# Kernel tuning notes

Measured on AMD Instinct MI355X. Metric: run time of the kernel, lower is better.

Reference implementation:

```python
import jax, jax.numpy as jnp
import numpy as np

DELTA = 2.5749
BN_EPS = 1e-5
N_LAYERS = 5


def _gin_pna_conv(x, src, dst, nW1, nb1, nW2, nb2, mW, mb):
    # x: [N, D]; src/dst: [E]
    N = x.shape[0]
    msgs = x[src]                                   # [E, D] gather (message = x_j)
    cnt = jax.ops.segment_sum(jnp.ones_like(dst, dtype=x.dtype), dst, num_segments=N)  # [N]
    c = jnp.maximum(cnt, 1.0)[:, None]              # guard isolated nodes
    sums = jax.ops.segment_sum(msgs, dst, num_segments=N)          # [N, D]
    maxs = jax.ops.segment_max(msgs, dst, num_segments=N)
    maxs = jnp.where(cnt[:, None] > 0, maxs, 0.0)   # empty segments -> 0 (torch_scatter behavior)
    means = sums / c
    sq_means = jax.ops.segment_sum(msgs * msgs, dst, num_segments=N) / c
    var = jax.nn.relu(sq_means - means * means)
    base = jnp.concatenate([sums, maxs, means, var], axis=1)        # [N, 4D]
    amp = (c / DELTA) * base                        # amplification scaler
    att = (DELTA / c) * base                        # attenuation scaler
    comb = jnp.concatenate([base, amp, att], axis=1)                # [N, 12D]
    agg = comb @ mW.T + mb                          # mlp: 12D -> D
    h = agg + x                                     # GIN: (1+eps)*x_r + aggr, eps=0
    h = jax.nn.relu(h @ nW1.T + nb1) @ nW2.T + nb2  # nn = Linear-ReLU-Linear
    return h


def _batchnorm(x, gamma, beta):
    mu = jnp.mean(x, axis=0)
    var = jnp.var(x, axis=0)
    return (x - mu) * jax.lax.rsqrt(var + BN_EPS) * gamma + beta


def setup_inputs() -> dict:
    key = jax.random.key(0)
    ks = jax.random.split(key, 12)
    N, E, D, G, OUT = 100000, 1600000, 64, 512, 16
    s = 0.05
    p = lambda k, shape: jax.random.normal(k, shape, dtype=jnp.float32) * s
    return {
        "x": jax.random.normal(ks[0], (N, D), dtype=jnp.float32),
        "edge_index": jax.random.randint(ks[1], (2, E), 0, N),
        "batch": jnp.sort(jax.random.randint(ks[2], (N,), 0, G)),
        "encW": p(ks[3], (D, D)), "encb": jnp.zeros((D,), jnp.float32),
        "nnW1": p(ks[4], (N_LAYERS, D, D)), "nnb1": jnp.zeros((N_LAYERS, D), jnp.float32),
        "nnW2": p(ks[5], (N_LAYERS, D, D)), "nnb2": jnp.zeros((N_LAYERS, D), jnp.float32),
        "mlpW": p(ks[6], (N_LAYERS, D, 12 * D)), "mlpb": jnp.zeros((N_LAYERS, D), jnp.float32),
        "bnG": jnp.ones((N_LAYERS, D), jnp.float32), "bnB": jnp.zeros((N_LAYERS, D), jnp.float32),
        "fc1W": p(ks[7], (D, D)), "fc1b": jnp.zeros((D,), jnp.float32),
        "fc2W": p(ks[8], (OUT, D)), "fc2b": jnp.zeros((OUT,), jnp.float32),
    }


def reference(x, edge_index, batch, encW, encb, nnW1, nnb1, nnW2, nnb2,
              mlpW, mlpb, bnG, bnB, fc1W, fc1b, fc2W, fc2b):
    NUM_GRAPHS = 512
    src, dst = edge_index[0], edge_index[1]
    h = x @ encW.T + encb                           # encoder
    for i in range(N_LAYERS):                       # fixed small layer loop
        h = jax.nn.relu(_gin_pna_conv(h, src, dst, nnW1[i], nnb1[i],
                                      nnW2[i], nnb2[i], mlpW[i], mlpb[i]))
        h = _batchnorm(h, bnG[i], bnB[i])
    g = jax.ops.segment_sum(h, batch, num_segments=NUM_GRAPHS)      # global_add_pool
    g = jax.nn.relu(g @ fc1W.T + fc1b)              # dropout is identity in eval mode
    return g @ fc2W.T + fc2b
```

## Files before the change

### kernel.cpp

```cpp
#include <hip/hip_runtime.h>
#include <hip/hip_bf16.h>
#include <hip/hip_fp16.h>

#define DELTA 2.5749f
#define BN_EPS 1e-5f

#define NBUCK 512
#define NBLK 128
#define ECAP 3584

typedef __attribute__((ext_vector_type(8))) _Float16 f16x8;
typedef __attribute__((ext_vector_type(2))) _Float16 f16x2;
typedef __attribute__((ext_vector_type(4))) float f32x4;

__device__ inline unsigned short f2h(float f) {
    union { _Float16 h; unsigned short u; } v;
    v.h = (_Float16)f;
    return v.u;
}


__global__ __launch_bounds__(256) void k_cnt(const int* __restrict__ dst,
                                             int* __restrict__ cnts,
                                             int E, int npb, int CS) {
    __shared__ int hist[NBUCK];
    int t = threadIdx.x;
    hist[t] = 0; hist[t + 256] = 0;
    __syncthreads();
    int s0 = blockIdx.x * CS, s1 = min(s0 + CS, E);
    for (int e = s0 + t; e < s1; e += 256)
        atomicAdd(&hist[dst[e] / npb], 1);
    __syncthreads();
    cnts[blockIdx.x * NBUCK + t] = hist[t];
    cnts[blockIdx.x * NBUCK + t + 256] = hist[t + 256];
}

__global__ void k_bscan1(const int* __restrict__ cnts, int* __restrict__ bases,
                         int* __restrict__ btot) {
    __shared__ int s[NBLK];
    int b = blockIdx.x, t = threadIdx.x;
    int v = cnts[t * NBUCK + b];
    s[t] = v; __syncthreads();
    for (int off = 1; off < NBLK; off <<= 1) {
        int x = (t >= off) ? s[t - off] : 0;
        __syncthreads();
        s[t] += x;
        __syncthreads();
    }
    bases[t * NBUCK + b] = s[t] - v;
    if (t == NBLK - 1) btot[b] = s[t];
}

__global__ void k_btops(const int* __restrict__ btot, int* __restrict__ bbase,
                        int* __restrict__ rowptr, int E, int N) {
    __shared__ int s[NBUCK];
    int t = threadIdx.x;
    int v = btot[t];
    s[t] = v; __syncthreads();
    for (int off = 1; off < NBUCK; off <<= 1) {
        int x = (t >= off) ? s[t - off] : 0;
        __syncthreads();
        s[t] += x;
        __syncthreads();
    }
    bbase[t] = s[t] - v;
    if (t == 0) rowptr[N] = E;
}

__global__ __launch_bounds__(256) void k_scat(const int* __restrict__ dst,
                                              const int* __restrict__ src,
                                              const int* __restrict__ bases,
                                              const int* __restrict__ bbase,
                                              int2* __restrict__ eDS,
                                              int E, int npb, int CS) {
    __shared__ int cur[NBUCK];
    int t = threadIdx.x;
    cur[t] = bbase[t] + bases[blockIdx.x * NBUCK + t];
    cur[t + 256] = bbase[t + 256] + bases[blockIdx.x * NBUCK + t + 256];
    __syncthreads();
    int s0 = blockIdx.x * CS, s1 = min(s0 + CS, E);
    for (int e = s0 + t; e < s1; e += 256) {
        int d = dst[e];
        int p = d / npb;
        int pos = atomicAdd(&cur[p], 1);
        eDS[pos] = make_int2(d, src[e]);
    }
}

__global__ __launch_bounds__(256) void k_csr(const int2* __restrict__ eDS,
                                             const int* __restrict__ bbase,
                                             const int* __restrict__ btot,
                                             int* __restrict__ rowptr,
                                             int* __restrict__ col,
                                             float* __restrict__ cnt,
                                             int npb, int N) {
    __shared__ int2 sE[ECAP];
    __shared__ int pre[256], sc[256];
    int b = blockIdx.x, t = threadIdx.x;
    int lo = b * npb;
    if (lo >= N) return;
    int nn = min(npb, N - lo);
    int base = bbase[b], n = btot[b];
    pre[t] = 0;
    __syncthreads();
    const int2* gE = eDS + base;
    for (int i = t; i < n; i += 256) {
        int2 e = gE[i];
        if (i < ECAP) sE[i] = e;
        atomicAdd(&pre[e.x - lo], 1);
    }
    __syncthreads();
    int deg = (t < nn) ? pre[t] : 0;
    sc[t] = deg; __syncthreads();
    for (int off = 1; off < 256; off <<= 1) {
        int x = (t >= off) ? sc[t - off] : 0;
        __syncthreads();
        sc[t] += x;
        __syncthreads();
    }
    int excl = sc[t] - deg;
    if (t < nn) {
        rowptr[lo + t] = base + excl;
        cnt[lo + t] = (float)(deg > 0 ? deg : 1);
    }
    __syncthreads();
    pre[t] = excl;
    __syncthreads();
    for (int i = t; i < n; i += 256) {
        int2 e = (i < ECAP) ? sE[i] : gE[i];
        int pos = atomicAdd(&pre[e.x - lo], 1);
        col[base + pos] = e.y;
    }
}

__global__ void k_castw_mlp(const float* __restrict__ w, unsigned short* __restrict__ o,
                            int total) {
    int i = blockIdx.x * 256 + threadIdx.x;
    if (i >= total) return;
    int lane = i & 63;
    int sc = (i >> 6) & 7;
    int tile = (i >> 9) % 12;
    int layer = i / (64 * 8 * 12);
    int r16 = lane & 15, quad = lane >> 4;
    int mat = tile >> 2, nt = tile & 3;
    const float* sp = w + (size_t)(layer * 64 + nt * 16 + r16) * 768
                        + mat * 256 + sc * 32 + quad * 8;
    unsigned short* op = o + (size_t)i * 8;
#pragma unroll
    for (int j = 0; j < 8; j++) op[j] = f2h(sp[j]);
}

__global__ void k_castw_nn(const float* __restrict__ w, unsigned short* __restrict__ o,
                           int total) {
    int i = blockIdx.x * 256 + threadIdx.x;
    if (i >= total) return;
    int lane = i & 63;
    int s = (i >> 6) & 1;
    int nt = (i >> 7) & 3;
    int layer = i >> 9;
    int r16 = lane & 15, quad = lane >> 4;
    const float* sp = w + (size_t)(layer * 64 + nt * 16 + r16) * 64 + s * 32 + quad * 8;
    unsigned short* op = o + (size_t)i * 8;
#pragma unroll
    for (int j = 0; j < 8; j++) op[j] = f2h(sp[j]);
}

#define ACC2(V)                                                            \
    do {                                                                   \
        mx = __builtin_elementwise_max(mx, V);                             \
        float x0 = (float)V[0], x1 = (float)V[1];                          \
        sa += x0; qa = fmaf(x0, x0, qa);                                   \
        sb += x1; qb = fmaf(x1, x1, qb);                                   \
    } while (0)

__global__ __launch_bounds__(256) void k_agg(const unsigned short* __restrict__ h16,
                                             const int* __restrict__ rowptr,
                                             const int* __restrict__ col,
                                             const float* __restrict__ bnstat,
                                             const float* __restrict__ gamma,
                                             const float* __restrict__ beta,
                                             float invN, int first,
                                             unsigned short* __restrict__ baseF,
                                             int N) {
    int t = threadIdx.x;
    int lane = t & 63;
    int half = lane >> 5;
    int fl = lane & 31;
    int node = blockIdx.x * 8 + (t >> 6) * 2 + half;
    if (node >= N) return;
    int fo2 = fl * 2;
    float scx, scy, shx, shy;
    if (first) {
        scx = 1.f; scy = 1.f; shx = 0.f; shy = 0.f;
    } else {
        float mu0 = bnstat[fo2] * invN, mu1 = bnstat[fo2 + 1] * invN;
        float v0 = bnstat[64 + fo2] * invN - mu0 * mu0;
        float v1 = bnstat[64 + fo2 + 1] * invN - mu1 * mu1;
        scx = rsqrtf(v0 + BN_EPS) * gamma[fo2];
        scy = rsqrtf(v1 + BN_EPS) * gamma[fo2 + 1];
        shx = beta[fo2] - mu0 * scx;
        shy = beta[fo2 + 1] - mu1 * scy;
    }
    const _Float16* hp = (const _Float16*)h16;
    int s0 = rowptr[node], s1 = rowptr[node + 1];
    int deg = s1 - s0;
    float sa = 0.f, sb = 0.f, qa = 0.f, qb = 0.f;
    f16x2 mx;
    mx[0] = (_Float16)(-65504.0f); mx[1] = (_Float16)(-65504.0f);
    const _Float16* hb = hp + fo2;
    int nfull = deg >> 3;

    f16x2 vA[8];
    int cN[8];
    if (nfull >= 1) {
        int cC[8];
        const int* cp = col + s0;
#pragma unroll
        for (int j = 0; j < 8; j++) cC[j] = cp[j];
        if (nfull >= 2) {
#pragma unroll
            for (int j = 0; j < 8; j++) cN[j] = cp[8 + j];
        }
#pragma unroll
        for (int j = 0; j < 8; j++) vA[j] = *(const f16x2*)(hb + ((size_t)(unsigned)cC[j] << 6));
    }
    for (int b = 1; b < nfull; b++) {
        int cNN[8];
        f16x2 vB[8];
        if (b + 1 < nfull) {
            const int* cp = col + s0 + (b + 1) * 8;
#pragma unroll
            for (int j = 0; j < 8; j++) cNN[j] = cp[j];
        }
#pragma unroll
        for (int j = 0; j < 8; j++) vB[j] = *(const f16x2*)(hb + ((size_t)(unsigned)cN[j] << 6));
#pragma unroll
        for (int j = 0; j < 8; j++) ACC2(vA[j]);
#pragma unroll
        for (int j = 0; j < 8; j++) { vA[j] = vB[j]; }
#pragma unroll
        for (int j = 0; j < 8; j++) { cN[j] = cNN[j]; }
    }
    if (nfull >= 1) {
#pragma unroll
        for (int j = 0; j < 8; j++) ACC2(vA[j]);
    }
    int tb = s0 + nfull * 8;
    int rem = s1 - tb;
    if (rem > 0) {
        int cT[8];
        f16x2 vT[8];
#pragma unroll
        for (int j = 0; j < 8; j++) {
            int idx = (tb + j < s1) ? (tb + j) : (s1 - 1);
            cT[j] = col[idx];
        }
#pragma unroll
        for (int j = 0; j < 8; j++) vT[j] = *(const f16x2*)(hb + ((size_t)(unsigned)cT[j] << 6));
#pragma unroll
        for (int j = 0; j < 8; j++) {
            if (j < rem) ACC2(vT[j]);
        }
    }

    float c = (float)(deg > 0 ? deg : 1);
    float ic = 1.f / c;
    float sum0, sum1, max0, max1, mean0, mean1, var0, var1;
    if (deg == 0) {
        sum0 = sum1 = max0 = max1 = mean0 = mean1 = var0 = var1 = 0.f;
    } else {
        sum0 = fmaf(scx, sa, c * shx);
        sum1 = fmaf(scy, sb, c * shy);
        max0 = fmaf(scx, (float)mx[0], shx);
        max1 = fmaf(scy, (float)mx[1], shy);
        float m0 = sa * ic, m1 = sb * ic;
        mean0 = fmaf(scx, m0, shx);
        mean1 = fmaf(scy, m1, shy);
        var0 = scx * scx * fmaxf(fmaf(-m0, m0, qa * ic), 0.f);
        var1 = scy * scy * fmaxf(fmaf(-m1, m1, qb * ic), 0.f);
    }
    size_t b = (size_t)node * 256 + fo2;
    ushort2 o;
    o.x = f2h(sum0); o.y = f2h(sum1);  *(ushort2*)(baseF + b) = o;
    o.x = f2h(max0); o.y = f2h(max1);  *(ushort2*)(baseF + b + 64) = o;
    o.x = f2h(mean0); o.y = f2h(mean1); *(ushort2*)(baseF + b + 128) = o;
    o.x = f2h(var0); o.y = f2h(var1);  *(ushort2*)(baseF + b + 192) = o;
}

__global__ __launch_bounds__(256) void k_mlp(const unsigned short* __restrict__ baseF,
                                             const float* __restrict__ cnt,
                                             const unsigned short* __restrict__ mW2,
                                             const float* __restrict__ mb,
                                             const unsigned short* __restrict__ hres16,
                                             const float* __restrict__ bnstatPrev,
                                             const float* __restrict__ gammaP,
                                             const float* __restrict__ betaP,
                                             float invN, int first,
                                             const unsigned short* __restrict__ w1F,
                                             const float* __restrict__ b1,
                                             const unsigned short* __restrict__ w2F,
                                             const float* __restrict__ b2,
                                             float* __restrict__ bnstat,
                                             unsigned short* __restrict__ hOut16, int N) {
    __shared__ char smem[36864];
    _Float16* bufA = (_Float16*)smem;
    _Float16* bufB = bufA + 128 * 72;
    float* red = (float*)bufB;

    int t = threadIdx.x;
    int wave = t >> 6, lane = t & 63;
    int r16 = lane & 15, quad = lane >> 4;
    int n0 = blockIdx.x * 128;
    int m0 = n0 + wave * 32;

    const _Float16* aptr0 = (const _Float16*)baseF + (size_t)(m0 + r16) * 256 + quad * 8;
    const _Float16* aptr1 = aptr0 + 16 * 256;
    const _Float16* mw = (const _Float16*)mW2 + lane * 8;
    f32x4 acc0[12], acc1[12];
#pragma unroll
    for (int i = 0; i < 12; i++) {
        acc0[i] = (f32x4){0.f, 0.f, 0.f, 0.f};
        acc1[i] = (f32x4){0.f, 0.f, 0.f, 0.f};
    }
    f16x8 aC0 = *(const f16x8*)(aptr0);
    f16x8 aC1 = *(const f16x8*)(aptr1);

#pragma unroll 1
    for (int sc = 0; sc < 8; sc++) {
        f16x8 aN0, aN1;
        if (sc < 7) {
            aN0 = *(const f16x8*)(aptr0 + (sc + 1) * 32);
            aN1 = *(const f16x8*)(aptr1 + (sc + 1) * 32);
        }
#pragma unroll
        for (int tile = 0; tile < 12; tile++) {
            f16x8 wB = *(const f16x8*)(mw + (tile * 8 + sc) * 512);
            acc0[tile] = __builtin_amdgcn_mfma_f32_16x16x32_f16(aC0, wB, acc0[tile], 0, 0, 0);
            acc1[tile] = __builtin_amdgcn_mfma_f32_16x16x32_f16(aC1, wB, acc1[tile], 0, 0, 0);
        }
        aC0 = aN0; aC1 = aN1;
    }

    {
        int nl = wave * 32 + (lane >> 1);
        int fo = (lane & 1) * 32;
        int gn = n0 + nl;
        uint4* dp = (uint4*)(bufA + nl * 72 + fo);
        if (gn < N) {
            const uint4* sp = (const uint4*)(hres16 + (size_t)gn * 64 + fo);
            dp[0] = sp[0]; dp[1] = sp[1]; dp[2] = sp[2]; dp[3] = sp[3];
        } else {
            uint4 z = make_uint4(0, 0, 0, 0);
            dp[0] = z; dp[1] = z; dp[2] = z; dp[3] = z;
        }
    }
    __builtin_amdgcn_wave_barrier();

    float scf[4], shf[4], mbv[4];
#pragma unroll
    for (int nt = 0; nt < 4; nt++) {
        int f = nt * 16 + r16;
        mbv[nt] = mb[f];
        if (first) {
            scf[nt] = 1.f; shf[nt] = 0.f;
        } else {
            float mu = bnstatPrev[f] * invN;
            float var = bnstatPrev[64 + f] * invN - mu * mu;
            float s = rsqrtf(var + BN_EPS) * gammaP[f];
            scf[nt] = s; shf[nt] = betaP[f] - mu * s;
        }
    }
#pragma unroll
    for (int mt = 0; mt < 2; mt++) {
#pragma unroll
        for (int i = 0; i < 4; i++) {
            int nl = wave * 32 + mt * 16 + quad * 4 + i;
            int gn = n0 + nl;
            if (gn < N) {
                float c = cnt[gn];
                float amp = c / DELTA, att = DELTA / c;
                f32x4* a = mt ? acc1 : acc0;
#pragma unroll
                for (int nt = 0; nt < 4; nt++) {
                    int f = nt * 16 + r16;
                    float r = (float)bufA[nl * 72 + f];
                    float v = a[nt][i] + amp * a[4 + nt][i] + att * a[8 + nt][i]
                            + mbv[nt] + fmaf(r, scf[nt], shf[nt]);
                    bufA[nl * 72 + f] = (_Float16)v;
                }
            }
        }
    }
    __builtin_amdgcn_wave_barrier();

    f32x4 accN[8];
#pragma unroll
    for (int i = 0; i < 8; i++) accN[i] = (f32x4){0.f, 0.f, 0.f, 0.f};
#pragma unroll
    for (int s = 0; s < 2; s++) {
        f16x8 fA0 = *(const f16x8*)(bufA + (wave * 32 + r16) * 72 + s * 32 + quad * 8);
        f16x8 fA1 = *(const f16x8*)(bufA + (wave * 32 + 16 + r16) * 72 + s * 32 + quad * 8);
#pragma unroll
        for (int nt = 0; nt < 4; nt++) {
            f16x8 wB = *(const f16x8*)((const _Float16*)w1F + ((nt * 2 + s) * 64 + lane) * 8);
            accN[nt]     = __builtin_amdgcn_mfma_f32_16x16x32_f16(fA0, wB, accN[nt], 0, 0, 0);
            accN[4 + nt] = __builtin_amdgcn_mfma_f32_16x16x32_f16(fA1, wB, accN[4 + nt], 0, 0, 0);
        }
    }
    float b1v[4];
#pragma unroll
    for (int nt = 0; nt < 4; nt++) b1v[nt] = b1[nt * 16 + r16];
#pragma unroll
    for (int mt = 0; mt < 2; mt++) {
#pragma unroll
        for (int i = 0; i < 4; i++) {
            int nl = wave * 32 + mt * 16 + quad * 4 + i;
#pragma unroll
            for (int nt = 0; nt < 4; nt++) {
                float v = fmaxf(accN[mt * 4 + nt][i] + b1v[nt], 0.f);
                bufB[nl * 72 + nt * 16 + r16] = (_Float16)v;
            }
        }
    }
    __builtin_amdgcn_wave_barrier();

    f32x4 accM[8];
#pragma unroll
    for (int i = 0; i < 8; i++) accM[i] = (f32x4){0.f, 0.f, 0.f, 0.f};
#pragma unroll
    for (int s = 0; s < 2; s++) {
        f16x8 fA0 = *(const f16x8*)(bufB + (wave * 32 + r16) * 72 + s * 32 + quad * 8);
        f16x8 fA1 = *(const f16x8*)(bufB + (wave * 32 + 16 + r16) * 72 + s * 32 + quad * 8);
#pragma unroll
        for (int nt = 0; nt < 4; nt++) {
            f16x8 wB = *(const f16x8*)((const _Float16*)w2F + ((nt * 2 + s) * 64 + lane) * 8);
            accM[nt]     = __builtin_amdgcn_mfma_f32_16x16x32_f16(fA0, wB, accM[nt], 0, 0, 0);
            accM[4 + nt] = __builtin_amdgcn_mfma_f32_16x16x32_f16(fA1, wB, accM[4 + nt], 0, 0, 0);
        }
    }
    float b2v[4], s1[4], s2[4];
#pragma unroll
    for (int nt = 0; nt < 4; nt++) {
        b2v[nt] = b2[nt * 16 + r16]; s1[nt] = 0.f; s2[nt] = 0.f;
    }
#pragma unroll
    for (int mt = 0; mt < 2; mt++) {
#pragma unroll
        for (int i = 0; i < 4; i++) {
            int nl = wave * 32 + mt * 16 + quad * 4 + i;
            bool ok = (n0 + nl) < N;
#pragma unroll
            for (int nt = 0; nt < 4; nt++) {
                float v = fmaxf(accM[mt * 4 + nt][i] + b2v[nt], 0.f);
                if (ok) { s1[nt] += v; s2[nt] = fmaf(v, v, s2[nt]); }
                bufA[nl * 72 + nt * 16 + r16] = (_Float16)v;
            }
        }
    }
    __builtin_amdgcn_wave_barrier();

    {
        int nl = wave * 32 + (lane >> 1);
        int fo = (lane & 1) * 32;
        int gn = n0 + nl;
        if (gn < N) {
            const uint4* sp = (const uint4*)(bufA + nl * 72 + fo);
            uint4* dp = (uint4*)(hOut16 + (size_t)gn * 64 + fo);
            dp[0] = sp[0]; dp[1] = sp[1]; dp[2] = sp[2]; dp[3] = sp[3];
        }
    }

    __syncthreads();
#pragma unroll
    for (int nt = 0; nt < 4; nt++) {
        int row = wave * 4 + quad;
        red[row * 64 + nt * 16 + r16] = s1[nt];
        red[1024 + row * 64 + nt * 16 + r16] = s2[nt];
    }
    __syncthreads();
    if (t < 128) {
        int d = t & 63, part = t >> 6;
        float tot = 0.f;
#pragma unroll
        for (int r = 0; r < 16; r++) tot += red[part * 1024 + r * 64 + d];
        atomicAdd(&bnstat[part * 64 + d], tot);
    }
}

#define FMA16(ACC0, ACC1, ACC2, ACC3, A, W)                                \
    do {                                                                   \
        ACC0.x = fmaf(A.x, W.x, ACC0.x); ACC0.y = fmaf(A.x, W.y, ACC0.y);  \
        ACC0.z = fmaf(A.x, W.z, ACC0.z); ACC0.w = fmaf(A.x, W.w, ACC0.w);  \
        ACC1.x = fmaf(A.y, W.x, ACC1.x); ACC1.y = fmaf(A.y, W.y, ACC1.y);  \
        ACC1.z = fmaf(A.y, W.z, ACC1.z); ACC1.w = fmaf(A.y, W.w, ACC1.w);  \
        ACC2.x = fmaf(A.z, W.x, ACC2.x); ACC2.y = fmaf(A.z, W.y, ACC2.y);  \
        ACC2.z = fmaf(A.z, W.z, ACC2.z); ACC2.w = fmaf(A.z, W.w, ACC2.w);  \
        ACC3.x = fmaf(A.w, W.x, ACC3.x); ACC3.y = fmaf(A.w, W.y, ACC3.y);  \
        ACC3.z = fmaf(A.w, W.z, ACC3.z); ACC3.w = fmaf(A.w, W.w, ACC3.w);  \
    } while (0)

__global__ __launch_bounds__(256) void k_gemm64(const float* __restrict__ in,
                                                const float* __restrict__ W,
                                                const float* __restrict__ bias,
                                                unsigned short* __restrict__ out16, int N) {
    __shared__ float sInT[64][64];
    __shared__ float sWT[64][64];
    int t = threadIdx.x;
    int tx = t & 15, ty = t >> 4;
    int n0 = blockIdx.x * 64;
    int c4 = tx * 4;
#pragma unroll
    for (int ch = 0; ch < 4; ch++) {
        int row = ch * 16 + ty;
        float4 v = make_float4(0.f, 0.f, 0.f, 0.f);
        if (n0 + row < N) v = *(const float4*)(in + (size_t)(n0 + row) * 64 + c4);
        sInT[c4 + 0][row] = v.x; sInT[c4 + 1][row] = v.y;
        sInT[c4 + 2][row] = v.z; sInT[c4 + 3][row] = v.w;
        float4 w = *(const float4*)(W + (size_t)row * 64 + c4);
        sWT[c4 + 0][row] = w.x; sWT[c4 + 1][row] = w.y;
        sWT[c4 + 2][row] = w.z; sWT[c4 + 3][row] = w.w;
    }
    __syncthreads();
    float4 acc0 = make_float4(0.f, 0.f, 0.f, 0.f);
    float4 acc1 = acc0, acc2 = acc0, acc3 = acc0;
#pragma unroll 8
    for (int k = 0; k < 64; k++) {
        float4 a = *(const float4*)(&sInT[k][ty * 4]);
        float4 w = *(const float4*)(&sWT[k][tx * 4]);
        FMA16(acc0, acc1, acc2, acc3, a, w);
    }
    float4 b4 = *(const float4*)(bias + tx * 4);
#pragma unroll
    for (int i = 0; i < 4; i++) {
        int n = n0 + ty * 4 + i;
        if (n < N) {
            float4 v = (i == 0) ? acc0 : (i == 1) ? acc1 : (i == 2) ? acc2 : acc3;
            v.x += b4.x; v.y += b4.y; v.z += b4.z; v.w += b4.w;
            ushort4 o;
            o.x = f2h(v.x); o.y = f2h(v.y); o.z = f2h(v.z); o.w = f2h(v.w);
            *(ushort4*)(out16 + (size_t)n * 64 + tx * 4) = o;
        }
    }
}

__global__ void k_pool(const unsigned short* __restrict__ h16, const int* __restrict__ batch,
                       const float* __restrict__ bnstat, const float* __restrict__ gamma,
                       const float* __restrict__ beta, float invN,
                       float* __restrict__ g, int N) {
    int d = threadIdx.x & 63, r = threadIdx.x >> 6;
    float mu = bnstat[d] * invN;
    float var = bnstat[64 + d] * invN - mu * mu;
    float sc = rsqrtf(var + BN_EPS) * gamma[d];
    float sh = beta[d] - mu * sc;
    const _Float16* hp = (const _Float16*)h16;
    int nbase = blockIdx.x * 32;
    float acc = 0.f;
    int gcur = -1;
    for (int i = 0; i < 8; i++) {
        int n = nbase + i * 4 + r;
        if (n < N) {
            int gb = batch[n];
            if (gb != gcur) {
                if (gcur >= 0) atomicAdd(&g[gcur * 64 + d], acc);
                acc = 0.f; gcur = gb;
            }
            acc += fmaf((float)hp[(size_t)n * 64 + d], sc, sh);
        }
    }
    if (gcur >= 0) atomicAdd(&g[gcur * 64 + d], acc);
}

__global__ void k_head(const float* __restrict__ g, const float* __restrict__ fc1W,
                       const float* __restrict__ fc1b, const float* __restrict__ fc2W,
                       const float* __restrict__ fc2b, float* __restrict__ out) {
    __shared__ float sg[64], sg1[64];
    int gi = blockIdx.x, t = threadIdx.x;
    sg[t] = g[gi * 64 + t];
    __syncthreads();
    float a = fc1b[t];
    for (int k = 0; k < 64; k++) a = fmaf(sg[k], fc1W[t * 64 + k], a);
    sg1[t] = fmaxf(a, 0.f);
    __syncthreads();
    if (t < 16) {
        float o = fc2b[t];
        for (int k = 0; k < 64; k++) o = fmaf(sg1[k], fc2W[t * 64 + k], o);
        out[gi * 16 + t] = o;
    }
}

extern "C" void kernel_launch(void* const* d_in, const int* in_sizes, int n_in,
                              void* d_out, int out_size, void* d_ws, size_t ws_size,
                              hipStream_t stream) {
    const float* x       = (const float*)d_in[0];
    const int*   eidx    = (const int*)d_in[1];
    const int*   batch   = (const int*)d_in[2];
    const float* encW    = (const float*)d_in[3];
    const float* encb    = (const float*)d_in[4];
    const float* nnW1    = (const float*)d_in[5];
    const float* nnb1    = (const float*)d_in[6];
    const float* nnW2    = (const float*)d_in[7];
    const float* nnb2    = (const float*)d_in[8];
    const float* mlpW    = (const float*)d_in[9];
    const float* mlpb    = (const float*)d_in[10];
    const float* bnG     = (const float*)d_in[11];
    const float* bnB     = (const float*)d_in[12];
    const float* fc1W    = (const float*)d_in[13];
    const float* fc1b    = (const float*)d_in[14];
    const float* fc2W    = (const float*)d_in[15];
    const float* fc2b    = (const float*)d_in[16];
    float* out = (float*)d_out;

    const int N = in_sizes[0] / 64;
    const int E = in_sizes[1] / 2;
    const int G = 512;
    const int* src = eidx;
    const int* dst = eidx + E;
    const int npb = (N + NBUCK - 1) / NBUCK;
    const float invN = 1.f / (float)N;
    const int CS = (E + NBLK - 1) / NBLK;

    char* ws = (char*)d_ws;
    size_t off = 0;
    auto alloc = [&](size_t bytes) { size_t r = off; off = (off + bytes + 255) & ~(size_t)255; return r; };
    int*   rowptr  = (int*)(ws + alloc((size_t)(N + 1) * 4));
    int*   col     = (int*)(ws + alloc((size_t)E * 4));
    int2*  eDS     = (int2*)(ws + alloc((size_t)E * 8));
    int*   cnts    = (int*)(ws + alloc((size_t)NBLK * NBUCK * 4));
    int*   bases   = (int*)(ws + alloc((size_t)NBLK * NBUCK * 4));
    int*   btot    = (int*)(ws + alloc(NBUCK * 4));
    int*   bbase   = (int*)(ws + alloc(NBUCK * 4));
    float* cnt     = (float*)(ws + alloc((size_t)N * 4));
    unsigned short* baseF = (unsigned short*)(ws + alloc((size_t)N * 256 * 2 + 131072));
    unsigned short* hC16 = (unsigned short*)(ws + alloc((size_t)N * 64 * 2 + 32768));
    unsigned short* mWF  = (unsigned short*)(ws + alloc((size_t)5 * 64 * 768 * 2));
    unsigned short* nW1F = (unsigned short*)(ws + alloc((size_t)5 * 64 * 64 * 2));
    unsigned short* nW2F = (unsigned short*)(ws + alloc((size_t)5 * 64 * 64 * 2));
    float* bnstats = (float*)(ws + alloc(5 * 128 * 4));
    float* gpool   = (float*)(ws + alloc((size_t)G * 64 * 4));

    hipMemsetAsync(bnstats, 0, 5 * 128 * 4, stream);
    hipMemsetAsync(gpool, 0, (size_t)G * 64 * 4, stream);

    int ngrid64 = (N + 63) / 64;
    int ngrid128 = (N + 127) / 128;

    k_cnt<<<NBLK, 256, 0, stream>>>(dst, cnts, E, npb, CS);
    k_bscan1<<<NBUCK, NBLK, 0, stream>>>(cnts, bases, btot);
    k_btops<<<1, NBUCK, 0, stream>>>(btot, bbase, rowptr, E, N);
    k_scat<<<NBLK, 256, 0, stream>>>(dst, src, bases, bbase, eDS, E, npb, CS);
    k_csr<<<NBUCK, 256, 0, stream>>>(eDS, bbase, btot, rowptr, col, cnt, npb, N);

    k_castw_mlp<<<120, 256, 0, stream>>>(mlpW, mWF, 30720);
    k_castw_nn<<<10, 256, 0, stream>>>(nnW1, nW1F, 2560);
    k_castw_nn<<<10, 256, 0, stream>>>(nnW2, nW2F, 2560);

    k_gemm64<<<ngrid64, 256, 0, stream>>>(x, encW, encb, hC16, N);

    for (int i = 0; i < 5; i++) {
        const float* bsPrev = (i == 0) ? bnstats : bnstats + (i - 1) * 128;
        const float* gP = (i == 0) ? bnG : bnG + (i - 1) * 64;
        const float* bP = (i == 0) ? bnB : bnB + (i - 1) * 64;
        int first = (i == 0) ? 1 : 0;
        k_agg<<<(N + 7) / 8, 256, 0, stream>>>(hC16, rowptr, col, bsPrev, gP, bP,
                                               invN, first, baseF, N);
        k_mlp<<<ngrid128, 256, 0, stream>>>(baseF, cnt,
                                            mWF + (size_t)i * 49152, mlpb + i * 64,
                                            hC16, bsPrev, gP, bP, invN, first,
                                            nW1F + (size_t)i * 4096, nnb1 + i * 64,
                                            nW2F + (size_t)i * 4096, nnb2 + i * 64,
                                            bnstats + i * 128, hC16, N);
    }

    k_pool<<<(N + 31) / 32, 256, 0, stream>>>(hC16, batch, bnstats + 4 * 128,
                                              bnG + 4 * 64, bnB + 4 * 64, invN, gpool, N);
    k_head<<<G, 64, 0, stream>>>(gpool, fc1W, fc1b, fc2W, fc2b, out);
}
```

Measured before the change: 716.5 us.

## Stage MLP weight slices through LDS and deepen A-operand prefetch

The weight cast kernel now lays out the fp16 MLP weights grouped by K-slice rather than by tile. The aggregation GEMM stages each 12KB slice cooperatively into shared memory with register double-buffering, instead of every wave reading weight fragments from global memory. The A-operand prefetch is also deepened to two slices ahead. This cuts redundant global and L2 weight traffic across waves, at the cost of extra shared memory (49KB per block, lowering occupancy) and two block barriers per K-slice.

```diff
diff --git a/kernel.cpp b/kernel.cpp
--- a/kernel.cpp
+++ b/kernel.cpp
@@ -138,9 +138,9 @@
     int i = blockIdx.x * 256 + threadIdx.x;
     if (i >= total) return;
     int lane = i & 63;
-    int sc = (i >> 6) & 7;
-    int tile = (i >> 9) % 12;
-    int layer = i / (64 * 8 * 12);
+    int tile = (i >> 6) % 12;
+    int sc = (i / 768) % 8;
+    int layer = i / 6144;
     int r16 = lane & 15, quad = lane >> 4;
     int mat = tile >> 2, nt = tile & 3;
     const float* sp = w + (size_t)(layer * 64 + nt * 16 + r16) * 768
@@ -302,10 +302,11 @@
                                              const float* __restrict__ b2,
                                              float* __restrict__ bnstat,
                                              unsigned short* __restrict__ hOut16, int N) {
-    __shared__ char smem[36864];
-    _Float16* bufA = (_Float16*)smem;
+    __shared__ char smem[49152];
+    _Float16* ldsW = (_Float16*)smem;
+    _Float16* bufA = (_Float16*)(smem + 12288);
     _Float16* bufB = bufA + 128 * 72;
-    float* red = (float*)bufB;
+    float* red = (float*)smem;
 
     int t = threadIdx.x;
     int wave = t >> 6, lane = t & 63;
@@ -315,30 +316,51 @@
 
     const _Float16* aptr0 = (const _Float16*)baseF + (size_t)(m0 + r16) * 256 + quad * 8;
     const _Float16* aptr1 = aptr0 + 16 * 256;
-    const _Float16* mw = (const _Float16*)mW2 + lane * 8;
     f32x4 acc0[12], acc1[12];
 #pragma unroll
     for (int i = 0; i < 12; i++) {
         acc0[i] = (f32x4){0.f, 0.f, 0.f, 0.f};
         acc1[i] = (f32x4){0.f, 0.f, 0.f, 0.f};
     }
+    uint4 st0, st1, st2;
+    {
+        const uint4* sp = (const uint4*)mW2;
+        st0 = sp[t]; st1 = sp[t + 256]; st2 = sp[t + 512];
+    }
     f16x8 aC0 = *(const f16x8*)(aptr0);
     f16x8 aC1 = *(const f16x8*)(aptr1);
+    f16x8 aN0 = *(const f16x8*)(aptr0 + 32);
+    f16x8 aN1 = *(const f16x8*)(aptr1 + 32);
+    {
+        uint4* dp = (uint4*)ldsW;
+        dp[t] = st0; dp[t + 256] = st1; dp[t + 512] = st2;
+    }
+    __syncthreads();
 
 #pragma unroll 1
     for (int sc = 0; sc < 8; sc++) {
-        f16x8 aN0, aN1;
         if (sc < 7) {
-            aN0 = *(const f16x8*)(aptr0 + (sc + 1) * 32);
-            aN1 = *(const f16x8*)(aptr1 + (sc + 1) * 32);
+            const uint4* sp = (const uint4*)(mW2 + (sc + 1) * 6144);
+            st0 = sp[t]; st1 = sp[t + 256]; st2 = sp[t + 512];
+        }
+        f16x8 aP0, aP1;
+        if (sc < 6) {
+            aP0 = *(const f16x8*)(aptr0 + (sc + 2) * 32);
+            aP1 = *(const f16x8*)(aptr1 + (sc + 2) * 32);
         }
 #pragma unroll
         for (int tile = 0; tile < 12; tile++) {
-            f16x8 wB = *(const f16x8*)(mw + (tile * 8 + sc) * 512);
-            acc0[tile] = __builtin_amdgcn_mfma_f32_16x16x32_f16(aC0, wB, acc0[tile], 0, 0, 0);
-            acc1[tile] = __builtin_amdgcn_mfma_f32_16x16x32_f16(aC1, wB, acc1[tile], 0, 0, 0);
-        }
-        aC0 = aN0; aC1 = aN1;
+            f16x8 wF = *(const f16x8*)(ldsW + tile * 512 + lane * 8);
+            acc0[tile] = __builtin_amdgcn_mfma_f32_16x16x32_f16(aC0, wF, acc0[tile], 0, 0, 0);
+            acc1[tile] = __builtin_amdgcn_mfma_f32_16x16x32_f16(aC1, wF, acc1[tile], 0, 0, 0);
+        }
+        if (sc < 7) {
+            __syncthreads();
+            uint4* dp = (uint4*)ldsW;
+            dp[t] = st0; dp[t + 256] = st1; dp[t + 512] = st2;
+            __syncthreads();
+        }
+        aC0 = aN0; aC1 = aN1; aN0 = aP0; aN1 = aP1;
     }
 
     {
```

New measurement: 653.0 us. 8.9% less time.
